# Kernel tuning notes

Hardware: AMD Instinct MI355X
Metric: run time of the kernel (lower is better)

## Reference

```python
import jax, jax.numpy as jnp
import numpy as np
from functools import partial

# Module hyperparameters (from init_kwargs)
T, C_IN, H, W_DIM = 128, 16, 64, 64
C_OUT, KH, KW = 64, 3, 3
PAD = ((1, 1), (1, 1))  # (top,bottom),(left,right) -> symmetric here
STRIDES = (1, 1)
F_V_THRESH = 8.0
F_V_THRESH_LOW = -1.0
F_V_RESET = 0.0
# fVSubtract is None -> reset-to-value branch


def setup_inputs() -> dict:
    key = jax.random.key(0)
    kx, kw, kb = jax.random.split(key, 3)
    x = jax.random.uniform(kx, (T, C_IN, H, W_DIM), dtype=jnp.float32)
    fan_in = C_IN * KH * KW
    bound = 1.0 / np.sqrt(fan_in)
    W = jax.random.uniform(kw, (C_OUT, C_IN, KH, KW), dtype=jnp.float32,
                           minval=-bound, maxval=bound)
    b = jax.random.uniform(kb, (C_OUT,), dtype=jnp.float32,
                           minval=-bound, maxval=bound)
    return {"x": x, "W": W, "b": b}


def _spiking_conv(x, W, b):
    # conv over all timesteps at once (time is the conv batch dim): [T, C_out, H, W]
    conv_out = jax.lax.conv_general_dilated(
        x, W, window_strides=STRIDES, padding=PAD,
        dimension_numbers=("NCHW", "OIHW", "NCHW"))
    conv_out = conv_out + b[None, :, None, None]

    def step(state, conv_t):
        state = state + conv_t
        spikes = (state >= F_V_THRESH).astype(conv_t.dtype)
        # reset-to-value branch (fVSubtract is None)
        state = spikes * F_V_RESET + state * (1.0 - spikes)
        # nn.Threshold(v, v): x if x > v else v
        state = jnp.where(state > F_V_THRESH_LOW, state, F_V_THRESH_LOW)
        return state, spikes

    init_state = jnp.zeros(conv_out.shape[1:], dtype=conv_out.dtype)
    _, num_spikes = jax.lax.scan(step, init_state, conv_out)
    return num_spikes  # [T, C_out, H, W] float (0/1)


def reference(x, W, b):
    return _spiking_conv(x, W, b)
```

## Files before the change

kernel.cpp:

```cpp
#include <hip/hip_runtime.h>

#define T_STEPS 128
#define CIN     16
#define HH      64
#define WW      64
#define COUT    64
#define HWSZ    (HH * WW)
#define CHW     (COUT * HWSZ)
#define XCHW    (CIN * HWSZ)

#define TILE    32
#define HALO    34
#define LSTR    36
#define PLANE   (HALO * LSTR)
#define NST     (CIN * HALO * HALO)
#define WBLK    40

typedef float vfloat4 __attribute__((ext_vector_type(4)));

__global__ void transpose_w(const float* __restrict__ W, float* __restrict__ Wtr) {
    int e = blockIdx.x * 256 + threadIdx.x;
    if (e >= COUT * CIN * 9) return;
    int co = e / (CIN * 9);
    int r  = e - co * (CIN * 9);
    int ci = r / 9;
    int k  = r - ci * 9;
    Wtr[((co >> 2) * CIN + ci) * WBLK + (co & 3) * 9 + k] = W[e];
}

__global__ __launch_bounds__(512, 4)
void spiking_conv_pass1(const float* __restrict__ x, const float* __restrict__ Wtr,
                        const float* __restrict__ b, float* __restrict__ out) {
    __shared__ float xs[CIN * PLANE];

    const int tid = threadIdx.x;
    const int t   = blockIdx.y;
    const int h0  = (blockIdx.x >> 1) * TILE;
    const int w0  = (blockIdx.x & 1) * TILE;

    const float* xt = x + t * XCHW;
    {
        float vbuf[19]; int ibuf[19];
#pragma unroll
        for (int k = 0; k < 18; ++k) {
            unsigned e = tid + k * 512;
            unsigned ci = e / (HALO * HALO);
            unsigned rem = e - ci * (HALO * HALO);
            unsigned r  = rem / HALO;
            unsigned c  = rem - r * HALO;
            int gh = h0 - 1 + (int)r;
            int gw = w0 - 1 + (int)c;
            bool inb = (unsigned)gh < HH && (unsigned)gw < WW;
            vbuf[k] = inb ? xt[ci * HWSZ + gh * WW + gw] : 0.f;
            ibuf[k] = ci * PLANE + r * LSTR + c;
        }
#pragma unroll
        for (int k = 0; k < 18; ++k) xs[ibuf[k]] = vbuf[k];
#pragma unroll
        for (int k = 0; k < 19; ++k) {
            unsigned e = tid + (18 + k) * 512;
            unsigned ci = e / (HALO * HALO);
            unsigned rem = e - ci * (HALO * HALO);
            unsigned r  = rem / HALO;
            unsigned c  = rem - r * HALO;
            int gh = h0 - 1 + (int)r;
            int gw = w0 - 1 + (int)c;
            bool inb = e < NST && (unsigned)gh < HH && (unsigned)gw < WW;
            vbuf[k] = inb ? xt[ci * HWSZ + gh * WW + gw] : 0.f;
            ibuf[k] = (e < NST) ? (int)(ci * PLANE + r * LSTR + c) : -1;
        }
#pragma unroll
        for (int k = 0; k < 19; ++k)
            if (ibuf[k] >= 0) xs[ibuf[k]] = vbuf[k];
    }
    __syncthreads();

    const int cog = __builtin_amdgcn_readfirstlane(tid >> 8);
    const int sp  = tid & 255;
    const int pr0 = sp >> 3;
    const int pc0 = (sp & 7) * 4;
    float* outt = out + t * CHW;

#pragma unroll 1
    for (int coh = 0; coh < 2; ++coh) {
        float acc[16][4];
#pragma unroll
        for (int j = 0; j < 16; ++j)
#pragma unroll
            for (int p = 0; p < 4; ++p) acc[j][p] = 0.f;

#pragma unroll 1
        for (int ci = 0; ci < CIN; ++ci) {
            float xv[3][6];
#pragma unroll
            for (int dr = 0; dr < 3; ++dr) {
                const float* row = &xs[ci * PLANE + (pr0 + dr) * LSTR + pc0];
                float4 a  = *(const float4*)row;
                float2 c2 = *(const float2*)(row + 4);
                xv[dr][0] = a.x;  xv[dr][1] = a.y;
                xv[dr][2] = a.z;  xv[dr][3] = a.w;
                xv[dr][4] = c2.x; xv[dr][5] = c2.y;
            }
#pragma unroll
            for (int g = 0; g < 4; ++g) {
                const int g4 = coh * 8 + cog * 4 + g;
                const float* wb = Wtr + (g4 * CIN + ci) * WBLK;
                float w[36];
#pragma unroll
                for (int i = 0; i < 36; ++i) w[i] = wb[i];
#pragma unroll
                for (int jj = 0; jj < 4; ++jj)
#pragma unroll
                    for (int ky = 0; ky < 3; ++ky)
#pragma unroll
                        for (int kx = 0; kx < 3; ++kx) {
                            const float wv = w[jj * 9 + ky * 3 + kx];
#pragma unroll
                            for (int p = 0; p < 4; ++p)
                                acc[g * 4 + jj][p] += wv * xv[ky][kx + p];
                        }
            }
        }

#pragma unroll
        for (int g = 0; g < 4; ++g)
#pragma unroll
            for (int jj = 0; jj < 4; ++jj) {
                const int co = coh * 32 + cog * 16 + g * 4 + jj;
                const float bias = b[co];
                float4 o;
                o.x = acc[g * 4 + jj][0] + bias;
                o.y = acc[g * 4 + jj][1] + bias;
                o.z = acc[g * 4 + jj][2] + bias;
                o.w = acc[g * 4 + jj][3] + bias;
                *(float4*)&outt[co * HWSZ + (h0 + pr0) * WW + (w0 + pc0)] = o;
            }
    }
}

__global__ __launch_bounds__(256)
void spiking_scan_pass2(const float* __restrict__ src, float* __restrict__ dst) {
    const int idx = blockIdx.x * 256 + threadIdx.x;
    const float4* ps = (const float4*)src + idx;
    vfloat4* pd = (vfloat4*)dst + idx;
    float sx = 0.f, sy = 0.f, sz = 0.f, sw = 0.f;
    float4 v[8], nv[8];
#pragma unroll
    for (int i = 0; i < 8; ++i) v[i] = ps[(size_t)i * (CHW / 4)];
#pragma unroll 1
    for (int tb = 0; tb < 15; ++tb) {
#pragma unroll
        for (int i = 0; i < 8; ++i) nv[i] = ps[(size_t)((tb + 1) * 8 + i) * (CHW / 4)];
#pragma unroll
        for (int i = 0; i < 8; ++i) {
            vfloat4 o;
            sx += v[i].x; bool a0 = (sx >= 8.0f); o.x = a0 ? 1.f : 0.f; sx = a0 ? 0.f : sx; sx = fmaxf(sx, -1.f);
            sy += v[i].y; bool a1 = (sy >= 8.0f); o.y = a1 ? 1.f : 0.f; sy = a1 ? 0.f : sy; sy = fmaxf(sy, -1.f);
            sz += v[i].z; bool a2 = (sz >= 8.0f); o.z = a2 ? 1.f : 0.f; sz = a2 ? 0.f : sz; sz = fmaxf(sz, -1.f);
            sw += v[i].w; bool a3 = (sw >= 8.0f); o.w = a3 ? 1.f : 0.f; sw = a3 ? 0.f : sw; sw = fmaxf(sw, -1.f);
            __builtin_nontemporal_store(o, &pd[(size_t)(tb * 8 + i) * (CHW / 4)]);
        }
#pragma unroll
        for (int i = 0; i < 8; ++i) v[i] = nv[i];
    }
#pragma unroll
    for (int i = 0; i < 8; ++i) {
        vfloat4 o;
        sx += v[i].x; bool a0 = (sx >= 8.0f); o.x = a0 ? 1.f : 0.f; sx = a0 ? 0.f : sx; sx = fmaxf(sx, -1.f);
        sy += v[i].y; bool a1 = (sy >= 8.0f); o.y = a1 ? 1.f : 0.f; sy = a1 ? 0.f : sy; sy = fmaxf(sy, -1.f);
        sz += v[i].z; bool a2 = (sz >= 8.0f); o.z = a2 ? 1.f : 0.f; sz = a2 ? 0.f : sz; sz = fmaxf(sz, -1.f);
        sw += v[i].w; bool a3 = (sw >= 8.0f); o.w = a3 ? 1.f : 0.f; sw = a3 ? 0.f : sw; sw = fmaxf(sw, -1.f);
        __builtin_nontemporal_store(o, &pd[(size_t)(120 + i) * (CHW / 4)]);
    }
}

extern "C" void kernel_launch(void* const* d_in, const int* in_sizes, int n_in,
                              void* d_out, int out_size, void* d_ws, size_t ws_size,
                              hipStream_t stream) {
    const float* x = (const float*)d_in[0];
    const float* W = (const float*)d_in[1];
    const float* b = (const float*)d_in[2];
    float* out = (float*)d_out;
    float* Wtr = (float*)d_ws;

    const size_t CONV_BYTES = (size_t)T_STEPS * CHW * sizeof(float);
    const size_t CONV_OFF   = 1u << 20;
    const bool   big_ws     = ws_size >= CONV_OFF + CONV_BYTES;
    float* conv = big_ws ? (float*)((char*)d_ws + CONV_OFF) : out;

    transpose_w<<<36, 256, 0, stream>>>(W, Wtr);

    dim3 g1(4, 128);
    spiking_conv_pass1<<<g1, 512, 0, stream>>>(x, Wtr, b, conv);

    spiking_scan_pass2<<<(CHW / 4) / 256, 256, 0, stream>>>(conv, out);
}
```

Baseline: 272.3 us.

## Halve conv spatial tile and retile threads to 8 pixels by 8 channels

The spatial tile for the conv pass shrinks from 32x32 to 16x32, so the launch uses twice as many blocks (8x128). The per-thread work mapping also changes: each wave now owns 8 output channels, and each lane computes 8 consecutive pixels in one pass, replacing the two-pass loop over 16 channels x 4 pixels. Each input row load is reused across more pixels, the block needs less shared memory, and the grid gives more parallelism. In exchange the halo overhead per tile grows and the weights are reread more often across blocks.

```diff
diff --git a/kernel.cpp b/kernel.cpp
--- a/kernel.cpp
+++ b/kernel.cpp
@@ -9,11 +9,13 @@
 #define CHW     (COUT * HWSZ)
 #define XCHW    (CIN * HWSZ)
 
-#define TILE    32
-#define HALO    34
+#define TILEH   16
+#define TILEW   32
+#define HALOH   18
+#define HALOW   34
 #define LSTR    36
-#define PLANE   (HALO * LSTR)
-#define NST     (CIN * HALO * HALO)
+#define PLANE   (HALOH * LSTR)
+#define NST     (CIN * HALOH * HALOW)
 #define WBLK    40
 
 typedef float vfloat4 __attribute__((ext_vector_type(4)));
@@ -35,19 +37,19 @@
 
     const int tid = threadIdx.x;
     const int t   = blockIdx.y;
-    const int h0  = (blockIdx.x >> 1) * TILE;
-    const int w0  = (blockIdx.x & 1) * TILE;
+    const int h0  = (blockIdx.x >> 1) * TILEH;
+    const int w0  = (blockIdx.x & 1) * TILEW;
 
     const float* xt = x + t * XCHW;
     {
-        float vbuf[19]; int ibuf[19];
-#pragma unroll
-        for (int k = 0; k < 18; ++k) {
+        float vbuf[10]; int ibuf[10];
+#pragma unroll
+        for (int k = 0; k < 10; ++k) {
             unsigned e = tid + k * 512;
-            unsigned ci = e / (HALO * HALO);
-            unsigned rem = e - ci * (HALO * HALO);
-            unsigned r  = rem / HALO;
-            unsigned c  = rem - r * HALO;
+            unsigned ci = e / (HALOH * HALOW);
+            unsigned rem = e - ci * (HALOH * HALOW);
+            unsigned r  = rem / HALOW;
+            unsigned c  = rem - r * HALOW;
             int gh = h0 - 1 + (int)r;
             int gw = w0 - 1 + (int)c;
             bool inb = (unsigned)gh < HH && (unsigned)gw < WW;
@@ -55,14 +57,14 @@
             ibuf[k] = ci * PLANE + r * LSTR + c;
         }
 #pragma unroll
-        for (int k = 0; k < 18; ++k) xs[ibuf[k]] = vbuf[k];
-#pragma unroll
-        for (int k = 0; k < 19; ++k) {
-            unsigned e = tid + (18 + k) * 512;
-            unsigned ci = e / (HALO * HALO);
-            unsigned rem = e - ci * (HALO * HALO);
-            unsigned r  = rem / HALO;
-            unsigned c  = rem - r * HALO;
+        for (int k = 0; k < 10; ++k) xs[ibuf[k]] = vbuf[k];
+#pragma unroll
+        for (int k = 0; k < 10; ++k) {
+            unsigned e = tid + (10 + k) * 512;
+            unsigned ci = e / (HALOH * HALOW);
+            unsigned rem = e - ci * (HALOH * HALOW);
+            unsigned r  = rem / HALOW;
+            unsigned c  = rem - r * HALOW;
             int gh = h0 - 1 + (int)r;
             int gw = w0 - 1 + (int)c;
             bool inb = e < NST && (unsigned)gh < HH && (unsigned)gw < WW;
@@ -70,72 +72,76 @@
             ibuf[k] = (e < NST) ? (int)(ci * PLANE + r * LSTR + c) : -1;
         }
 #pragma unroll
-        for (int k = 0; k < 19; ++k)
+        for (int k = 0; k < 10; ++k)
             if (ibuf[k] >= 0) xs[ibuf[k]] = vbuf[k];
     }
     __syncthreads();
 
-    const int cog = __builtin_amdgcn_readfirstlane(tid >> 8);
-    const int sp  = tid & 255;
-    const int pr0 = sp >> 3;
-    const int pc0 = (sp & 7) * 4;
+    const int cog = __builtin_amdgcn_readfirstlane(tid >> 6);
+    const int ln  = tid & 63;
+    const int pr0 = ln >> 2;
+    const int pc0 = (ln & 3) * 8;
     float* outt = out + t * CHW;
 
+    float acc[8][8];
+#pragma unroll
+    for (int j = 0; j < 8; ++j)
+#pragma unroll
+        for (int p = 0; p < 8; ++p) acc[j][p] = 0.f;
+
 #pragma unroll 1
-    for (int coh = 0; coh < 2; ++coh) {
-        float acc[16][4];
-#pragma unroll
-        for (int j = 0; j < 16; ++j)
-#pragma unroll
-            for (int p = 0; p < 4; ++p) acc[j][p] = 0.f;
-
-#pragma unroll 1
-        for (int ci = 0; ci < CIN; ++ci) {
-            float xv[3][6];
-#pragma unroll
-            for (int dr = 0; dr < 3; ++dr) {
-                const float* row = &xs[ci * PLANE + (pr0 + dr) * LSTR + pc0];
-                float4 a  = *(const float4*)row;
-                float2 c2 = *(const float2*)(row + 4);
-                xv[dr][0] = a.x;  xv[dr][1] = a.y;
-                xv[dr][2] = a.z;  xv[dr][3] = a.w;
-                xv[dr][4] = c2.x; xv[dr][5] = c2.y;
-            }
-#pragma unroll
-            for (int g = 0; g < 4; ++g) {
-                const int g4 = coh * 8 + cog * 4 + g;
-                const float* wb = Wtr + (g4 * CIN + ci) * WBLK;
-                float w[36];
-#pragma unroll
-                for (int i = 0; i < 36; ++i) w[i] = wb[i];
-#pragma unroll
-                for (int jj = 0; jj < 4; ++jj)
-#pragma unroll
-                    for (int ky = 0; ky < 3; ++ky)
-#pragma unroll
-                        for (int kx = 0; kx < 3; ++kx) {
-                            const float wv = w[jj * 9 + ky * 3 + kx];
-#pragma unroll
-                            for (int p = 0; p < 4; ++p)
-                                acc[g * 4 + jj][p] += wv * xv[ky][kx + p];
-                        }
-            }
-        }
-
-#pragma unroll
-        for (int g = 0; g < 4; ++g)
-#pragma unroll
-            for (int jj = 0; jj < 4; ++jj) {
-                const int co = coh * 32 + cog * 16 + g * 4 + jj;
-                const float bias = b[co];
-                float4 o;
-                o.x = acc[g * 4 + jj][0] + bias;
-                o.y = acc[g * 4 + jj][1] + bias;
-                o.z = acc[g * 4 + jj][2] + bias;
-                o.w = acc[g * 4 + jj][3] + bias;
-                *(float4*)&outt[co * HWSZ + (h0 + pr0) * WW + (w0 + pc0)] = o;
-            }
-    }
+    for (int ci = 0; ci < CIN; ++ci) {
+        float xv[3][10];
+#pragma unroll
+        for (int dr = 0; dr < 3; ++dr) {
+            const float* row = &xs[ci * PLANE + (pr0 + dr) * LSTR + pc0];
+            float4 a  = *(const float4*)row;
+            float4 b4 = *(const float4*)(row + 4);
+            float2 c2 = *(const float2*)(row + 8);
+            xv[dr][0] = a.x;  xv[dr][1] = a.y;  xv[dr][2] = a.z;  xv[dr][3] = a.w;
+            xv[dr][4] = b4.x; xv[dr][5] = b4.y; xv[dr][6] = b4.z; xv[dr][7] = b4.w;
+            xv[dr][8] = c2.x; xv[dr][9] = c2.y;
+        }
+#pragma unroll
+        for (int g = 0; g < 2; ++g) {
+            const int g4 = cog * 2 + g;
+            const float* wb = Wtr + (g4 * CIN + ci) * WBLK;
+            float w[36];
+#pragma unroll
+            for (int i = 0; i < 36; ++i) w[i] = wb[i];
+#pragma unroll
+            for (int jj = 0; jj < 4; ++jj)
+#pragma unroll
+                for (int ky = 0; ky < 3; ++ky)
+#pragma unroll
+                    for (int kx = 0; kx < 3; ++kx) {
+                        const float wv = w[jj * 9 + ky * 3 + kx];
+#pragma unroll
+                        for (int p = 0; p < 8; ++p)
+                            acc[g * 4 + jj][p] += wv * xv[ky][kx + p];
+                    }
+        }
+    }
+
+#pragma unroll
+    for (int g = 0; g < 2; ++g)
+#pragma unroll
+        for (int jj = 0; jj < 4; ++jj) {
+            const int co = cog * 8 + g * 4 + jj;
+            const float bias = b[co];
+            float* op = &outt[co * HWSZ + (h0 + pr0) * WW + (w0 + pc0)];
+            float4 o0, o1;
+            o0.x = acc[g * 4 + jj][0] + bias;
+            o0.y = acc[g * 4 + jj][1] + bias;
+            o0.z = acc[g * 4 + jj][2] + bias;
+            o0.w = acc[g * 4 + jj][3] + bias;
+            o1.x = acc[g * 4 + jj][4] + bias;
+            o1.y = acc[g * 4 + jj][5] + bias;
+            o1.z = acc[g * 4 + jj][6] + bias;
+            o1.w = acc[g * 4 + jj][7] + bias;
+            *(float4*)op = o0;
+            *(float4*)(op + 4) = o1;
+        }
 }
 
 __global__ __launch_bounds__(256)
@@ -190,7 +196,7 @@
 
     transpose_w<<<36, 256, 0, stream>>>(W, Wtr);
 
-    dim3 g1(4, 128);
+    dim3 g1(8, 128);
     spiking_conv_pass1<<<g1, 512, 0, stream>>>(x, Wtr, b, conv);
 
     spiking_scan_pass2<<<(CHW / 4) / 256, 256, 0, stream>>>(conv, out);
```

Result: faster. 257.6 us (-5.4%).
